# Kernel tuning notes

Measured on AMD Instinct MI355X. Metric: run time of the kernel, lower is better.

Reference implementation:

```python
import jax, jax.numpy as jnp
import numpy as np

B, N, T = 32, 256, 1024  # batch, num_dimensions, time_dur


def setup_inputs() -> dict:
    key = jax.random.key(0)
    k1, k2 = jax.random.split(key)
    x = jax.random.normal(k1, (B, N, T), dtype=jnp.float32)
    # DBNN.__init__: tau_rise=50, tau_decay=200, omega=2 (all per-dimension)
    tau_rise = jnp.full((N,), 50.0, dtype=jnp.float32)
    tau_decay = jnp.full((N,), 200.0, dtype=jnp.float32)
    omega = jnp.full((N,), 2.0, dtype=jnp.float32)
    # BilinearModified weight: uniform(-1/sqrt(N), 1/sqrt(N)), shape [out=1, N, N]
    bound = 1.0 / np.sqrt(N)
    W = jax.random.uniform(k2, (1, N, N), minval=-bound, maxval=bound, dtype=jnp.float32)
    return {"x": x, "tau_rise": tau_rise, "tau_decay": tau_decay, "omega": omega, "W": W}


def reference(x, tau_rise, tau_decay, omega, W):
    B_, N_, T_ = x.shape
    BIAS = -70.0  # fixed bias buffer in BilinearModified

    # --- create_kernels: [N, T] exponential rise/decay kernels ---
    t = jnp.arange(T_, dtype=x.dtype)
    kernels = (omega[:, None]
               * (1.0 - jnp.exp(-t / tau_rise[:, None]))
               * jnp.exp(-t / tau_decay[:, None]))  # [N, T]

    # torch flips the kernel then runs cross-correlation (conv1d) => causal convolution
    k_flipped = jnp.flip(kernels, axis=-1)[:, None, :]  # [N, 1, T] (OIW, depthwise)

    y = jax.lax.conv_general_dilated(
        x, k_flipped,
        window_strides=(1,),
        padding=[(T_ - 1, T_ - 1)],
        dimension_numbers=("NCH", "OIH", "NCH"),
        feature_group_count=N_,
    )[:, :, :T_]  # [B, N, T]

    yt = jnp.transpose(y, (0, 2, 1))  # [B, T, N]

    # Bilinear with diagonal of weight zeroed (mask-multiply, equivalent to the
    # in-place diagonal-zeroing loop in the torch module)
    Wm = W * (1.0 - jnp.eye(N_, dtype=W.dtype))  # [1, N, N]
    bilinear = jnp.einsum("btn,onm,btm->bto", yt, Wm, yt)  # [B, T, 1]

    linear = jnp.sum(yt, axis=2, keepdims=True)  # [B, T, 1]
    out = bilinear + BIAS + linear
    return out[..., 0]  # [B, T]
```

## Files before the change

kernel.cpp:

```cpp
#include <hip/hip_runtime.h>

typedef _Float16 f16;
typedef _Float16 f16x4 __attribute__((ext_vector_type(4)));
typedef _Float16 f16x8 __attribute__((ext_vector_type(8)));
typedef float    f32x4 __attribute__((ext_vector_type(4)));

#define NB 32
#define ND 256
#define NT 1024

__global__ __launch_bounds__(256) void iir_wprep_kernel(
    const float* __restrict__ x, const float* __restrict__ tau_rise,
    const float* __restrict__ tau_decay, const float* __restrict__ omega,
    const float* __restrict__ W, f16* __restrict__ y16, f16* __restrict__ wf)
{
    if (blockIdx.x >= 2048) {
        const int gid  = (blockIdx.x - 2048) * 256 + threadIdx.x;
        const int kh   = gid >> 12;
        const int ks   = (gid >> 10) & 3;
        const int nt   = (gid >> 6) & 15;
        const int lane = gid & 63;
        const int nrow = nt * 16 + (lane & 15);
        const int k0   = kh * 128 + ks * 32 + (lane >> 4) * 8;
        f16x8 v;
        #pragma unroll
        for (int j = 0; j < 8; ++j) {
            int k = k0 + j;
            float w = W[nrow * 256 + k];
            v[j] = (f16)((k == nrow) ? 0.0f : w);
        }
        *reinterpret_cast<f16x8*>(wf + (size_t)gid * 8) = v;
        return;
    }

    const int lane = threadIdx.x & 63;
    const int wid  = threadIdx.x >> 6;
    const int row  = blockIdx.x * 4 + wid;
    const int n    = row & (ND - 1);

    const float td = tau_decay[n];
    const float tr = tau_rise[n];
    const float om = omega[n];
    const float ad = expf(-1.0f / td);
    const float am = expf(-(1.0f / tr + 1.0f / td));

    const float* xr = x + (size_t)row * NT + lane * 16;
    float xv[16];
    #pragma unroll
    for (int i = 0; i < 4; ++i) {
        f32x4 v = *reinterpret_cast<const f32x4*>(xr + i * 4);
        xv[i*4+0] = v[0]; xv[i*4+1] = v[1]; xv[i*4+2] = v[2]; xv[i*4+3] = v[3];
    }

    float ld[16], lm[16];
    float sd = 0.f, sm = 0.f;
    #pragma unroll
    for (int i = 0; i < 16; ++i) {
        sd = fmaf(ad, sd, xv[i]); ld[i] = sd;
        sm = fmaf(am, sm, xv[i]); lm[i] = sm;
    }

    float t2;
    t2 = ad * ad; t2 = t2 * t2; t2 = t2 * t2; const float a16d = t2 * t2;
    t2 = am * am; t2 = t2 * t2; t2 = t2 * t2; const float a16m = t2 * t2;

    float Xd = sd, Xm = sm;
    float wdp = a16d, wmp = a16m;
    #pragma unroll
    for (int off = 1; off < 64; off <<= 1) {
        float pd = __shfl_up(Xd, off);
        float pm = __shfl_up(Xm, off);
        if (lane >= off) { Xd = fmaf(wdp, pd, Xd); Xm = fmaf(wmp, pm, Xm); }
        wdp *= wdp; wmp *= wmp;
    }
    float cd = __shfl_up(Xd, 1);
    float cm = __shfl_up(Xm, 1);
    if (lane == 0) { cd = 0.f; cm = 0.f; }

    f16x8 o0, o1;
    float pd = ad, pm = am;
    #pragma unroll
    for (int i = 0; i < 16; ++i) {
        float yd = fmaf(pd, cd, ld[i]);
        float ym = fmaf(pm, cm, lm[i]);
        float yv = om * (yd - ym);
        if (i < 8) o0[i] = (f16)yv; else o1[i - 8] = (f16)yv;
        pd *= ad; pm *= am;
    }
    f16* dst = y16 + (size_t)row * NT + lane * 16;
    *reinterpret_cast<f16x8*>(dst)     = o0;
    *reinterpret_cast<f16x8*>(dst + 8) = o1;
}

__global__ __launch_bounds__(512, 1) void bilinear_kernel(
    const f16* __restrict__ y16, const f16* __restrict__ wf,
    float* __restrict__ out)
{
    __shared__ __align__(16) f16 Wl[32768];
    __shared__ __align__(16) f16 Yl[32768];
    __shared__ float sbuf[4][128];

    const int bi = blockIdx.x;
    const int tt = bi & 7;
    const int b  = bi >> 3;
    const int t0 = tt * 128;
    const int tid = threadIdx.x;

    const int m    = tid & 255;
    const int half = tid >> 8;
    const f16* ysrc = y16 + ((size_t)(b * ND + m)) * NT + t0 + half * 64;
    f16x8 vy[8];
    #pragma unroll
    for (int c = 0; c < 8; ++c)
        vy[c] = *reinterpret_cast<const f16x8*>(ysrc + c * 8);

    f16x8 vw[8];
    #pragma unroll
    for (int k = 0; k < 8; ++k)
        vw[k] = *reinterpret_cast<const f16x8*>(&wf[(size_t)(k * 512 + tid) * 8]);

    #pragma unroll
    for (int c = 0; c < 8; ++c) {
        #pragma unroll
        for (int e = 0; e < 8; ++e) {
            int tl = half * 64 + c * 8 + e;
            Yl[tl * 256 + (m ^ (e << 3))] = vy[c][e];
        }
    }
    #pragma unroll
    for (int k = 0; k < 8; ++k)
        *reinterpret_cast<f16x8*>(&Wl[(k * 512 + tid) * 8]) = vw[k];
    #pragma unroll
    for (int k = 0; k < 8; ++k)
        vw[k] = *reinterpret_cast<const f16x8*>(
            &wf[(size_t)(32768 / 8 + k * 512 + tid) * 8]);

    const int lane = tid & 63;
    const int w    = tid >> 6;
    const int wt   = w >> 2;
    const int wn   = w & 3;
    const int g    = lane >> 4;

    int tl4[4], sw4[4];
    #pragma unroll
    for (int tf = 0; tf < 4; ++tf) {
        tl4[tf] = wt * 64 + tf * 16 + (lane & 15);
        sw4[tf] = (tl4[tf] & 7) << 3;
    }

    f32x4 acc[4][4];
    #pragma unroll
    for (int a = 0; a < 4; ++a)
        #pragma unroll
        for (int tf = 0; tf < 4; ++tf) acc[a][tf] = (f32x4){0.f,0.f,0.f,0.f};

    #pragma unroll
    for (int kh = 0; kh < 2; ++kh) {
        __syncthreads();
        if (kh == 1) {
            #pragma unroll
            for (int k = 0; k < 8; ++k)
                *reinterpret_cast<f16x8*>(&Wl[(k * 512 + tid) * 8]) = vw[k];
            __syncthreads();
        }
        #pragma unroll
        for (int ks = 0; ks < 4; ++ks) {
            f16x8 bfrag[4];
            #pragma unroll
            for (int tf = 0; tf < 4; ++tf) {
                int m0 = kh * 128 + ks * 32 + g * 8;
                bfrag[tf] = *reinterpret_cast<const f16x8*>(
                    &Yl[tl4[tf] * 256 + (m0 ^ sw4[tf])]);
            }
            #pragma unroll
            for (int a = 0; a < 4; ++a) {
                int nt = wn * 4 + a;
                f16x8 afrag = *reinterpret_cast<const f16x8*>(
                    &Wl[((ks * 16 + nt) * 64 + lane) * 8]);
                #pragma unroll
                for (int tf = 0; tf < 4; ++tf)
                    acc[a][tf] = __builtin_amdgcn_mfma_f32_16x16x32_f16(
                        afrag, bfrag[tf], acc[a][tf], 0, 0, 0);
            }
        }
    }

    #pragma unroll
    for (int tf = 0; tf < 4; ++tf) {
        float p = 0.f;
        #pragma unroll
        for (int a = 0; a < 4; ++a) {
            int n0 = (wn * 4 + a) * 16 + g * 4;
            f16x4 yv4 = *reinterpret_cast<const f16x4*>(
                &Yl[tl4[tf] * 256 + (n0 ^ sw4[tf])]);
            #pragma unroll
            for (int r = 0; r < 4; ++r)
                p = fmaf((float)yv4[r], acc[a][tf][r] + 1.0f, p);
        }
        p += __shfl_xor(p, 16);
        p += __shfl_xor(p, 32);
        if (lane < 16) sbuf[wn][wt * 64 + tf * 16 + lane] = p;
    }
    __syncthreads();
    if (tid < 128) {
        out[b * NT + t0 + tid] =
            sbuf[0][tid] + sbuf[1][tid] + sbuf[2][tid] + sbuf[3][tid] - 70.0f;
    }
}

extern "C" void kernel_launch(void* const* d_in, const int* in_sizes, int n_in,
                              void* d_out, int out_size, void* d_ws, size_t ws_size,
                              hipStream_t stream) {
    const float* x         = (const float*)d_in[0];
    const float* tau_rise  = (const float*)d_in[1];
    const float* tau_decay = (const float*)d_in[2];
    const float* omega     = (const float*)d_in[3];
    const float* W         = (const float*)d_in[4];
    float* out = (float*)d_out;

    f16* y16 = (f16*)d_ws;
    f16* wfr = (f16*)((char*)d_ws + (size_t)16 * 1024 * 1024);

    iir_wprep_kernel<<<2048 + 32, 256, 0, stream>>>(
        x, tau_rise, tau_decay, omega, W, y16, wfr);
    bilinear_kernel<<<NB * 8, 512, 0, stream>>>(y16, wfr, out);
}
```

Baseline: 24.37 us.

## Fuse IIR scan and bilinear MFMA into one cooperative kernel with grid sync

```diff
diff --git a/kernel.cpp b/kernel.cpp
--- a/kernel.cpp
+++ b/kernel.cpp
@@ -1,4 +1,7 @@
 #include <hip/hip_runtime.h>
+#include <hip/hip_cooperative_groups.h>
+
+namespace cg = cooperative_groups;
 
 typedef _Float16 f16;
 typedef _Float16 f16x4 __attribute__((ext_vector_type(4)));
@@ -9,202 +12,217 @@
 #define ND 256
 #define NT 1024
 
-__global__ __launch_bounds__(256) void iir_wprep_kernel(
+__global__ __launch_bounds__(512, 1) void dbnn_fused_kernel(
     const float* __restrict__ x, const float* __restrict__ tau_rise,
     const float* __restrict__ tau_decay, const float* __restrict__ omega,
-    const float* __restrict__ W, f16* __restrict__ y16, f16* __restrict__ wf)
-{
-    if (blockIdx.x >= 2048) {
-        const int gid  = (blockIdx.x - 2048) * 256 + threadIdx.x;
-        const int kh   = gid >> 12;
-        const int ks   = (gid >> 10) & 3;
-        const int nt   = (gid >> 6) & 15;
-        const int lane = gid & 63;
-        const int nrow = nt * 16 + (lane & 15);
-        const int k0   = kh * 128 + ks * 32 + (lane >> 4) * 8;
-        f16x8 v;
-        #pragma unroll
-        for (int j = 0; j < 8; ++j) {
-            int k = k0 + j;
-            float w = W[nrow * 256 + k];
-            v[j] = (f16)((k == nrow) ? 0.0f : w);
-        }
-        *reinterpret_cast<f16x8*>(wf + (size_t)gid * 8) = v;
-        return;
-    }
-
-    const int lane = threadIdx.x & 63;
-    const int wid  = threadIdx.x >> 6;
-    const int row  = blockIdx.x * 4 + wid;
-    const int n    = row & (ND - 1);
-
-    const float td = tau_decay[n];
-    const float tr = tau_rise[n];
-    const float om = omega[n];
-    const float ad = expf(-1.0f / td);
-    const float am = expf(-(1.0f / tr + 1.0f / td));
-
-    const float* xr = x + (size_t)row * NT + lane * 16;
-    float xv[16];
-    #pragma unroll
-    for (int i = 0; i < 4; ++i) {
-        f32x4 v = *reinterpret_cast<const f32x4*>(xr + i * 4);
-        xv[i*4+0] = v[0]; xv[i*4+1] = v[1]; xv[i*4+2] = v[2]; xv[i*4+3] = v[3];
-    }
-
-    float ld[16], lm[16];
-    float sd = 0.f, sm = 0.f;
-    #pragma unroll
-    for (int i = 0; i < 16; ++i) {
-        sd = fmaf(ad, sd, xv[i]); ld[i] = sd;
-        sm = fmaf(am, sm, xv[i]); lm[i] = sm;
-    }
-
-    float t2;
-    t2 = ad * ad; t2 = t2 * t2; t2 = t2 * t2; const float a16d = t2 * t2;
-    t2 = am * am; t2 = t2 * t2; t2 = t2 * t2; const float a16m = t2 * t2;
-
-    float Xd = sd, Xm = sm;
-    float wdp = a16d, wmp = a16m;
-    #pragma unroll
-    for (int off = 1; off < 64; off <<= 1) {
-        float pd = __shfl_up(Xd, off);
-        float pm = __shfl_up(Xm, off);
-        if (lane >= off) { Xd = fmaf(wdp, pd, Xd); Xm = fmaf(wmp, pm, Xm); }
-        wdp *= wdp; wmp *= wmp;
-    }
-    float cd = __shfl_up(Xd, 1);
-    float cm = __shfl_up(Xm, 1);
-    if (lane == 0) { cd = 0.f; cm = 0.f; }
-
-    f16x8 o0, o1;
-    float pd = ad, pm = am;
-    #pragma unroll
-    for (int i = 0; i < 16; ++i) {
-        float yd = fmaf(pd, cd, ld[i]);
-        float ym = fmaf(pm, cm, lm[i]);
-        float yv = om * (yd - ym);
-        if (i < 8) o0[i] = (f16)yv; else o1[i - 8] = (f16)yv;
-        pd *= ad; pm *= am;
-    }
-    f16* dst = y16 + (size_t)row * NT + lane * 16;
-    *reinterpret_cast<f16x8*>(dst)     = o0;
-    *reinterpret_cast<f16x8*>(dst + 8) = o1;
-}
-
-__global__ __launch_bounds__(512, 1) void bilinear_kernel(
-    const f16* __restrict__ y16, const f16* __restrict__ wf,
+    const float* __restrict__ W, f16* __restrict__ y16, f16* __restrict__ wf,
     float* __restrict__ out)
 {
     __shared__ __align__(16) f16 Wl[32768];
     __shared__ __align__(16) f16 Yl[32768];
     __shared__ float sbuf[4][128];
 
-    const int bi = blockIdx.x;
-    const int tt = bi & 7;
-    const int b  = bi >> 3;
-    const int t0 = tt * 128;
-    const int tid = threadIdx.x;
-
-    const int m    = tid & 255;
-    const int half = tid >> 8;
-    const f16* ysrc = y16 + ((size_t)(b * ND + m)) * NT + t0 + half * 64;
-    f16x8 vy[8];
-    #pragma unroll
-    for (int c = 0; c < 8; ++c)
-        vy[c] = *reinterpret_cast<const f16x8*>(ysrc + c * 8);
-
-    f16x8 vw[8];
-    #pragma unroll
-    for (int k = 0; k < 8; ++k)
-        vw[k] = *reinterpret_cast<const f16x8*>(&wf[(size_t)(k * 512 + tid) * 8]);
-
-    #pragma unroll
-    for (int c = 0; c < 8; ++c) {
-        #pragma unroll
-        for (int e = 0; e < 8; ++e) {
-            int tl = half * 64 + c * 8 + e;
-            Yl[tl * 256 + (m ^ (e << 3))] = vy[c][e];
-        }
-    }
-    #pragma unroll
-    for (int k = 0; k < 8; ++k)
-        *reinterpret_cast<f16x8*>(&Wl[(k * 512 + tid) * 8]) = vw[k];
-    #pragma unroll
-    for (int k = 0; k < 8; ++k)
-        vw[k] = *reinterpret_cast<const f16x8*>(
-            &wf[(size_t)(32768 / 8 + k * 512 + tid) * 8]);
-
+    const int tid  = threadIdx.x;
     const int lane = tid & 63;
     const int w    = tid >> 6;
-    const int wt   = w >> 2;
-    const int wn   = w & 3;
-    const int g    = lane >> 4;
-
-    int tl4[4], sw4[4];
-    #pragma unroll
-    for (int tf = 0; tf < 4; ++tf) {
-        tl4[tf] = wt * 64 + tf * 16 + (lane & 15);
-        sw4[tf] = (tl4[tf] & 7) << 3;
+
+    if (tid < 32) {
+        const int gid  = blockIdx.x * 32 + tid;
+        const int kh   = gid >> 12;
+        const int ks   = (gid >> 10) & 3;
+        const int nt   = (gid >> 6) & 15;
+        const int ln   = gid & 63;
+        const int nrow = nt * 16 + (ln & 15);
+        const int k0   = kh * 128 + ks * 32 + (ln >> 4) * 8;
+        f16x8 v;
+        #pragma unroll
+        for (int j = 0; j < 8; ++j) {
+            int k = k0 + j;
+            float wv = W[nrow * 256 + k];
+            v[j] = (f16)((k == nrow) ? 0.0f : wv);
+        }
+        *reinterpret_cast<f16x8*>(wf + (size_t)gid * 8) = v;
     }
 
-    f32x4 acc[4][4];
-    #pragma unroll
-    for (int a = 0; a < 4; ++a)
-        #pragma unroll
-        for (int tf = 0; tf < 4; ++tf) acc[a][tf] = (f32x4){0.f,0.f,0.f,0.f};
-
-    #pragma unroll
-    for (int kh = 0; kh < 2; ++kh) {
+    {
+        const int row0 = blockIdx.x * 32 + w * 4;
+        const float* xp = x + (size_t)row0 * NT + lane * 16;
+
+        f32x4 pre[4];
+        #pragma unroll
+        for (int i = 0; i < 4; ++i)
+            pre[i] = *reinterpret_cast<const f32x4*>(xp + i * 4);
+
+        #pragma unroll
+        for (int r = 0; r < 4; ++r) {
+            float xv[16];
+            #pragma unroll
+            for (int i = 0; i < 4; ++i) {
+                xv[i*4+0] = pre[i][0]; xv[i*4+1] = pre[i][1];
+                xv[i*4+2] = pre[i][2]; xv[i*4+3] = pre[i][3];
+            }
+            if (r < 3) {
+                xp += NT;
+                #pragma unroll
+                for (int i = 0; i < 4; ++i)
+                    pre[i] = *reinterpret_cast<const f32x4*>(xp + i * 4);
+            }
+
+            const int row = row0 + r;
+            const int n   = row & (ND - 1);
+            const float td = tau_decay[n];
+            const float tr = tau_rise[n];
+            const float om = omega[n];
+            const float ad = expf(-1.0f / td);
+            const float am = expf(-(1.0f / tr + 1.0f / td));
+
+            float ld[16], lm[16];
+            float sd = 0.f, sm = 0.f;
+            #pragma unroll
+            for (int i = 0; i < 16; ++i) {
+                sd = fmaf(ad, sd, xv[i]); ld[i] = sd;
+                sm = fmaf(am, sm, xv[i]); lm[i] = sm;
+            }
+
+            float t2;
+            t2 = ad*ad; t2 = t2*t2; t2 = t2*t2; const float a16d = t2*t2;
+            t2 = am*am; t2 = t2*t2; t2 = t2*t2; const float a16m = t2*t2;
+
+            float Xd = sd, Xm = sm;
+            float wdp = a16d, wmp = a16m;
+            #pragma unroll
+            for (int off = 1; off < 64; off <<= 1) {
+                float pd = __shfl_up(Xd, off);
+                float pm = __shfl_up(Xm, off);
+                if (lane >= off) { Xd = fmaf(wdp, pd, Xd); Xm = fmaf(wmp, pm, Xm); }
+                wdp *= wdp; wmp *= wmp;
+            }
+            float cd = __shfl_up(Xd, 1);
+            float cm = __shfl_up(Xm, 1);
+            if (lane == 0) { cd = 0.f; cm = 0.f; }
+
+            f16x8 o0, o1;
+            float pd = ad, pm = am;
+            #pragma unroll
+            for (int i = 0; i < 16; ++i) {
+                float yd = fmaf(pd, cd, ld[i]);
+                float ym = fmaf(pm, cm, lm[i]);
+                float yv = om * (yd - ym);
+                if (i < 8) o0[i] = (f16)yv; else o1[i - 8] = (f16)yv;
+                pd *= ad; pm *= am;
+            }
+            f16* dst = y16 + (size_t)row * NT + lane * 16;
+            *reinterpret_cast<f16x8*>(dst)     = o0;
+            *reinterpret_cast<f16x8*>(dst + 8) = o1;
+        }
+    }
+
+    cg::this_grid().sync();
+
+    {
+        const int bi = blockIdx.x;
+        const int tt = bi & 7;
+        const int b  = bi >> 3;
+        const int t0 = tt * 128;
+
+        const int m    = tid & 255;
+        const int half = tid >> 8;
+        const f16* ysrc = y16 + ((size_t)(b * ND + m)) * NT + t0 + half * 64;
+        f16x8 vy[8];
+        #pragma unroll
+        for (int c = 0; c < 8; ++c)
+            vy[c] = *reinterpret_cast<const f16x8*>(ysrc + c * 8);
+
+        f16x8 vw[8];
+        #pragma unroll
+        for (int k = 0; k < 8; ++k)
+            vw[k] = *reinterpret_cast<const f16x8*>(&wf[(size_t)(k * 512 + tid) * 8]);
+
+        #pragma unroll
+        for (int c = 0; c < 8; ++c) {
+            #pragma unroll
+            for (int e = 0; e < 8; ++e) {
+                int tl = half * 64 + c * 8 + e;
+                Yl[tl * 256 + (m ^ (e << 3))] = vy[c][e];
+            }
+        }
+        #pragma unroll
+        for (int k = 0; k < 8; ++k)
+            *reinterpret_cast<f16x8*>(&Wl[(k * 512 + tid) * 8]) = vw[k];
+        #pragma unroll
+        for (int k = 0; k < 8; ++k)
+            vw[k] = *reinterpret_cast<const f16x8*>(
+                &wf[(size_t)(32768 / 8 + k * 512 + tid) * 8]);
+
+        const int wt = w >> 2;
+        const int wn = w & 3;
+        const int g  = lane >> 4;
+
+        int tl4[4], sw4[4];
+        #pragma unroll
+        for (int tf = 0; tf < 4; ++tf) {
+            tl4[tf] = wt * 64 + tf * 16 + (lane & 15);
+            sw4[tf] = (tl4[tf] & 7) << 3;
+        }
+
+        f32x4 acc[4][4];
+        #pragma unroll
+        for (int a = 0; a < 4; ++a)
+            #pragma unroll
+            for (int tf = 0; tf < 4; ++tf) acc[a][tf] = (f32x4){0.f,0.f,0.f,0.f};
+
+        #pragma unroll
+        for (int kh = 0; kh < 2; ++kh) {
+            __syncthreads();
+            if (kh == 1) {
+                #pragma unroll
+                for (int k = 0; k < 8; ++k)
+                    *reinterpret_cast<f16x8*>(&Wl[(k * 512 + tid) * 8]) = vw[k];
+                __syncthreads();
+            }
+            #pragma unroll
+            for (int ks = 0; ks < 4; ++ks) {
+                f16x8 bfrag[4];
+                #pragma unroll
+                for (int tf = 0; tf < 4; ++tf) {
+                    int m0 = kh * 128 + ks * 32 + g * 8;
+                    bfrag[tf] = *reinterpret_cast<const f16x8*>(
+                        &Yl[tl4[tf] * 256 + (m0 ^ sw4[tf])]);
+                }
+                #pragma unroll
+                for (int a = 0; a < 4; ++a) {
+                    int nt = wn * 4 + a;
+                    f16x8 afrag = *reinterpret_cast<const f16x8*>(
+                        &Wl[((ks * 16 + nt) * 64 + lane) * 8]);
+                    #pragma unroll
+                    for (int tf = 0; tf < 4; ++tf)
+                        acc[a][tf] = __builtin_amdgcn_mfma_f32_16x16x32_f16(
+                            afrag, bfrag[tf], acc[a][tf], 0, 0, 0);
+                }
+            }
+        }
+
+        #pragma unroll
+        for (int tf = 0; tf < 4; ++tf) {
+            float p = 0.f;
+            #pragma unroll
+            for (int a = 0; a < 4; ++a) {
+                int n0 = (wn * 4 + a) * 16 + g * 4;
+                f16x4 yv4 = *reinterpret_cast<const f16x4*>(
+                    &Yl[tl4[tf] * 256 + (n0 ^ sw4[tf])]);
+                #pragma unroll
+                for (int r = 0; r < 4; ++r)
+                    p = fmaf((float)yv4[r], acc[a][tf][r] + 1.0f, p);
+            }
+            p += __shfl_xor(p, 16);
+            p += __shfl_xor(p, 32);
+            if (lane < 16) sbuf[wn][wt * 64 + tf * 16 + lane] = p;
+        }
         __syncthreads();
-        if (kh == 1) {
-            #pragma unroll
-            for (int k = 0; k < 8; ++k)
-                *reinterpret_cast<f16x8*>(&Wl[(k * 512 + tid) * 8]) = vw[k];
-            __syncthreads();
-        }
-        #pragma unroll
-        for (int ks = 0; ks < 4; ++ks) {
-            f16x8 bfrag[4];
-            #pragma unroll
-            for (int tf = 0; tf < 4; ++tf) {
-                int m0 = kh * 128 + ks * 32 + g * 8;
-                bfrag[tf] = *reinterpret_cast<const f16x8*>(
-                    &Yl[tl4[tf] * 256 + (m0 ^ sw4[tf])]);
-            }
-            #pragma unroll
-            for (int a = 0; a < 4; ++a) {
-                int nt = wn * 4 + a;
-                f16x8 afrag = *reinterpret_cast<const f16x8*>(
-                    &Wl[((ks * 16 + nt) * 64 + lane) * 8]);
-                #pragma unroll
-                for (int tf = 0; tf < 4; ++tf)
-                    acc[a][tf] = __builtin_amdgcn_mfma_f32_16x16x32_f16(
-                        afrag, bfrag[tf], acc[a][tf], 0, 0, 0);
-            }
-        }
-    }
-
-    #pragma unroll
-    for (int tf = 0; tf < 4; ++tf) {
-        float p = 0.f;
-        #pragma unroll
-        for (int a = 0; a < 4; ++a) {
-            int n0 = (wn * 4 + a) * 16 + g * 4;
-            f16x4 yv4 = *reinterpret_cast<const f16x4*>(
-                &Yl[tl4[tf] * 256 + (n0 ^ sw4[tf])]);
-            #pragma unroll
-            for (int r = 0; r < 4; ++r)
-                p = fmaf((float)yv4[r], acc[a][tf][r] + 1.0f, p);
-        }
-        p += __shfl_xor(p, 16);
-        p += __shfl_xor(p, 32);
-        if (lane < 16) sbuf[wn][wt * 64 + tf * 16 + lane] = p;
-    }
-    __syncthreads();
-    if (tid < 128) {
-        out[b * NT + t0 + tid] =
-            sbuf[0][tid] + sbuf[1][tid] + sbuf[2][tid] + sbuf[3][tid] - 70.0f;
+        if (tid < 128) {
+            out[b * NT + t0 + tid] =
+                sbuf[0][tid] + sbuf[1][tid] + sbuf[2][tid] + sbuf[3][tid] - 70.0f;
+        }
     }
 }
 
@@ -221,7 +239,10 @@
     f16* y16 = (f16*)d_ws;
     f16* wfr = (f16*)((char*)d_ws + (size_t)16 * 1024 * 1024);
 
-    iir_wprep_kernel<<<2048 + 32, 256, 0, stream>>>(
-        x, tau_rise, tau_decay, omega, W, y16, wfr);
-    bilinear_kernel<<<NB * 8, 512, 0, stream>>>(y16, wfr, out);
+    void* kargs[] = {
+        (void*)&x, (void*)&tau_rise, (void*)&tau_decay, (void*)&omega,
+        (void*)&W, (void*)&y16, (void*)&wfr, (void*)&out
+    };
+    hipLaunchCooperativeKernel((const void*)dbnn_fused_kernel,
+                               dim3(256), dim3(512), kargs, 0, stream);
 }
```

Result: slower. 71.22 us (+192.2%).

## Shrink bilinear tile, stream W fragments from global, raise occupancy

Applied to the files above, without the earlier changes.

```diff
diff --git a/kernel.cpp b/kernel.cpp
--- a/kernel.cpp
+++ b/kernel.cpp
@@ -16,12 +16,11 @@
 {
     if (blockIdx.x >= 2048) {
         const int gid  = (blockIdx.x - 2048) * 256 + threadIdx.x;
-        const int kh   = gid >> 12;
-        const int ks   = (gid >> 10) & 3;
+        const int ks8  = gid >> 10;
         const int nt   = (gid >> 6) & 15;
         const int lane = gid & 63;
         const int nrow = nt * 16 + (lane & 15);
-        const int k0   = kh * 128 + ks * 32 + (lane >> 4) * 8;
+        const int k0   = ks8 * 32 + (lane >> 4) * 8;
         f16x8 v;
         #pragma unroll
         for (int j = 0; j < 8; ++j) {
@@ -92,105 +91,83 @@
     *reinterpret_cast<f16x8*>(dst + 8) = o1;
 }
 
-__global__ __launch_bounds__(512, 1) void bilinear_kernel(
+__global__ __launch_bounds__(512, 4) void bilinear_kernel(
     const f16* __restrict__ y16, const f16* __restrict__ wf,
     float* __restrict__ out)
 {
-    __shared__ __align__(16) f16 Wl[32768];
-    __shared__ __align__(16) f16 Yl[32768];
-    __shared__ float sbuf[4][128];
+    __shared__ __align__(16) f16 Yl[16384];
+    __shared__ float sbuf[8][64];
 
     const int bi = blockIdx.x;
-    const int tt = bi & 7;
-    const int b  = bi >> 3;
-    const int t0 = tt * 128;
+    const int tt = bi & 15;
+    const int b  = bi >> 4;
+    const int t0 = tt * 64;
     const int tid = threadIdx.x;
 
-    const int m    = tid & 255;
-    const int half = tid >> 8;
-    const f16* ysrc = y16 + ((size_t)(b * ND + m)) * NT + t0 + half * 64;
-    f16x8 vy[8];
-    #pragma unroll
-    for (int c = 0; c < 8; ++c)
-        vy[c] = *reinterpret_cast<const f16x8*>(ysrc + c * 8);
-
-    f16x8 vw[8];
-    #pragma unroll
-    for (int k = 0; k < 8; ++k)
-        vw[k] = *reinterpret_cast<const f16x8*>(&wf[(size_t)(k * 512 + tid) * 8]);
-
-    #pragma unroll
-    for (int c = 0; c < 8; ++c) {
-        #pragma unroll
-        for (int e = 0; e < 8; ++e) {
-            int tl = half * 64 + c * 8 + e;
-            Yl[tl * 256 + (m ^ (e << 3))] = vy[c][e];
-        }
-    }
-    #pragma unroll
-    for (int k = 0; k < 8; ++k)
-        *reinterpret_cast<f16x8*>(&Wl[(k * 512 + tid) * 8]) = vw[k];
-    #pragma unroll
-    for (int k = 0; k < 8; ++k)
-        vw[k] = *reinterpret_cast<const f16x8*>(
-            &wf[(size_t)(32768 / 8 + k * 512 + tid) * 8]);
+    {
+        const int m    = tid & 255;
+        const int half = tid >> 8;
+        const f16* ysrc = y16 + ((size_t)(b * ND + m)) * NT + t0 + half * 32;
+        f16x8 vy[4];
+        #pragma unroll
+        for (int c = 0; c < 4; ++c)
+            vy[c] = *reinterpret_cast<const f16x8*>(ysrc + c * 8);
+        #pragma unroll
+        for (int c = 0; c < 4; ++c) {
+            #pragma unroll
+            for (int e = 0; e < 8; ++e) {
+                int tl = half * 32 + c * 8 + e;
+                Yl[tl * 256 + (m ^ (e << 3))] = vy[c][e];
+            }
+        }
+    }
+    __syncthreads();
 
     const int lane = tid & 63;
     const int w    = tid >> 6;
-    const int wt   = w >> 2;
-    const int wn   = w & 3;
     const int g    = lane >> 4;
 
     int tl4[4], sw4[4];
     #pragma unroll
     for (int tf = 0; tf < 4; ++tf) {
-        tl4[tf] = wt * 64 + tf * 16 + (lane & 15);
+        tl4[tf] = tf * 16 + (lane & 15);
         sw4[tf] = (tl4[tf] & 7) << 3;
     }
 
-    f32x4 acc[4][4];
-    #pragma unroll
-    for (int a = 0; a < 4; ++a)
+    f32x4 acc[2][4];
+    #pragma unroll
+    for (int a = 0; a < 2; ++a)
         #pragma unroll
         for (int tf = 0; tf < 4; ++tf) acc[a][tf] = (f32x4){0.f,0.f,0.f,0.f};
 
     #pragma unroll
-    for (int kh = 0; kh < 2; ++kh) {
-        __syncthreads();
-        if (kh == 1) {
+    for (int ks = 0; ks < 8; ++ks) {
+        f16x8 afrag[2];
+        #pragma unroll
+        for (int a = 0; a < 2; ++a)
+            afrag[a] = *reinterpret_cast<const f16x8*>(
+                &wf[(size_t)(((ks * 16) + (2 * w + a)) * 64 + lane) * 8]);
+        f16x8 bfrag[4];
+        #pragma unroll
+        for (int tf = 0; tf < 4; ++tf) {
+            int m0 = ks * 32 + g * 8;
+            bfrag[tf] = *reinterpret_cast<const f16x8*>(
+                &Yl[tl4[tf] * 256 + (m0 ^ sw4[tf])]);
+        }
+        #pragma unroll
+        for (int a = 0; a < 2; ++a)
             #pragma unroll
-            for (int k = 0; k < 8; ++k)
-                *reinterpret_cast<f16x8*>(&Wl[(k * 512 + tid) * 8]) = vw[k];
-            __syncthreads();
-        }
-        #pragma unroll
-        for (int ks = 0; ks < 4; ++ks) {
-            f16x8 bfrag[4];
-            #pragma unroll
-            for (int tf = 0; tf < 4; ++tf) {
-                int m0 = kh * 128 + ks * 32 + g * 8;
-                bfrag[tf] = *reinterpret_cast<const f16x8*>(
-                    &Yl[tl4[tf] * 256 + (m0 ^ sw4[tf])]);
-            }
-            #pragma unroll
-            for (int a = 0; a < 4; ++a) {
-                int nt = wn * 4 + a;
-                f16x8 afrag = *reinterpret_cast<const f16x8*>(
-                    &Wl[((ks * 16 + nt) * 64 + lane) * 8]);
-                #pragma unroll
-                for (int tf = 0; tf < 4; ++tf)
-                    acc[a][tf] = __builtin_amdgcn_mfma_f32_16x16x32_f16(
-                        afrag, bfrag[tf], acc[a][tf], 0, 0, 0);
-            }
-        }
+            for (int tf = 0; tf < 4; ++tf)
+                acc[a][tf] = __builtin_amdgcn_mfma_f32_16x16x32_f16(
+                    afrag[a], bfrag[tf], acc[a][tf], 0, 0, 0);
     }
 
     #pragma unroll
     for (int tf = 0; tf < 4; ++tf) {
         float p = 0.f;
         #pragma unroll
-        for (int a = 0; a < 4; ++a) {
-            int n0 = (wn * 4 + a) * 16 + g * 4;
+        for (int a = 0; a < 2; ++a) {
+            int n0 = w * 32 + a * 16 + g * 4;
             f16x4 yv4 = *reinterpret_cast<const f16x4*>(
                 &Yl[tl4[tf] * 256 + (n0 ^ sw4[tf])]);
             #pragma unroll
@@ -199,12 +176,13 @@
         }
         p += __shfl_xor(p, 16);
         p += __shfl_xor(p, 32);
-        if (lane < 16) sbuf[wn][wt * 64 + tf * 16 + lane] = p;
+        if (lane < 16) sbuf[w][tf * 16 + lane] = p;
     }
     __syncthreads();
-    if (tid < 128) {
-        out[b * NT + t0 + tid] =
-            sbuf[0][tid] + sbuf[1][tid] + sbuf[2][tid] + sbuf[3][tid] - 70.0f;
+    if (tid < 64) {
+        float s = sbuf[0][tid] + sbuf[1][tid] + sbuf[2][tid] + sbuf[3][tid]
+                + sbuf[4][tid] + sbuf[5][tid] + sbuf[6][tid] + sbuf[7][tid];
+        out[b * NT + t0 + tid] = s - 70.0f;
     }
 }
 
@@ -223,5 +201,5 @@
 
     iir_wprep_kernel<<<2048 + 32, 256, 0, stream>>>(
         x, tau_rise, tau_decay, omega, W, y16, wfr);
-    bilinear_kernel<<<NB * 8, 512, 0, stream>>>(y16, wfr, out);
+    bilinear_kernel<<<NB * 16, 512, 0, stream>>>(y16, wfr, out);
 }
```

Result: no change. 24.08 us (-1.2%).
